# Kernel optimization log

Measured on AMD Instinct MI355X. Metric: run time of the kernel, lower is better.

Reference implementation:

```python
import jax, jax.numpy as jnp
import numpy as np

H = 8
DK = 16  # 128 // 8
DM = 128


def setup_inputs() -> dict:
    key = jax.random.key(0)
    ks = jax.random.split(key, 12)
    B, S = 4, 2048
    inp = {
        "query": jax.random.normal(ks[0], (B, S, DM), dtype=jnp.float32),
        "key": jax.random.normal(ks[1], (B, S, DM), dtype=jnp.float32),
        "value": jax.random.normal(ks[2], (B, S, DM), dtype=jnp.float32),
        "pos_embed": jax.random.normal(ks[3], (B, S, DM), dtype=jnp.float32),
        # three projection linears (shared: L0 for pos_query & query, L1 for pos_key & key, L2 for value)
        "W0": jax.random.normal(ks[4], (DM, DM), dtype=jnp.float32) / np.sqrt(DM),
        "b0": jnp.zeros((DM,), dtype=jnp.float32),
        "W1": jax.random.normal(ks[5], (DM, DM), dtype=jnp.float32) / np.sqrt(DM),
        "b1": jnp.zeros((DM,), dtype=jnp.float32),
        "W2": jax.random.normal(ks[6], (DM, DM), dtype=jnp.float32) / np.sqrt(DM),
        "b2": jnp.zeros((DM,), dtype=jnp.float32),
        "Wo": jax.random.normal(ks[7], (DM, DM), dtype=jnp.float32) / np.sqrt(DM),
        "bo": jnp.zeros((DM,), dtype=jnp.float32),
    }
    return inp


def _proj(x, W, b):
    # Linear then split heads: [B,S,128] -> [B,H,S,DK]
    B = x.shape[0]
    y = x @ W.T + b
    return y.reshape(B, -1, H, DK).transpose(0, 2, 1, 3)


def reference(query, key, value, pos_embed, W0, b0, W1, b1, W2, b2, Wo, bo):
    B = query.shape[0]
    pos1 = pos_embed[..., 0:DM]
    pos_q = _proj(pos1, W0, b0)  # shares L0 with query proj (as in source zip bug)
    pos_k = _proj(pos1, W1, b1)
    pos_attn = jnp.einsum("bhqd,bhkd->bhqk", pos_q, pos_k)  # [B,H,S,S]

    q = _proj(query, W0, b0)
    k = _proj(key, W1, b1)
    v = _proj(value, W2, b2)

    scale = 1.0 / jnp.sqrt(jnp.asarray(DK, dtype=q.dtype))
    scores = jnp.einsum("bhqd,bhkd->bhqk", q, k) * scale + pos_attn
    attn = jax.nn.softmax(scores, axis=-1)  # dropout = identity (eval)
    x = jnp.einsum("bhqk,bhkd->bhqd", attn, v)  # [B,H,S,DK]
    x = x.transpose(0, 2, 1, 3).reshape(B, -1, H * DK)
    return x @ Wo.T + bo
```

## Files before the change

kernel.cpp:

```cpp
#include <hip/hip_runtime.h>
#include <math.h>

#define LOG2E 1.44269504088896340736f

typedef __attribute__((ext_vector_type(8))) short bfrag;
typedef __attribute__((ext_vector_type(4))) float f4;
typedef unsigned __attribute__((ext_vector_type(2))) u2;

__device__ __forceinline__ unsigned pk_trunc(float a, float b) {
    return (__float_as_uint(a) >> 16) | (__float_as_uint(b) & 0xFFFF0000u);
}
__device__ __forceinline__ unsigned pk_rne(float a, float b) {
    unsigned ua = __float_as_uint(a); ua += 0x7FFFu + ((ua >> 16) & 1u);
    unsigned ub = __float_as_uint(b); ub += 0x7FFFu + ((ub >> 16) & 1u);
    return (ua >> 16) | (ub & 0xFFFF0000u);
}
__device__ __forceinline__ float trunchi(float x) {
    return __uint_as_float(__float_as_uint(x) & 0xFFFF0000u);
}
__device__ __forceinline__ float fexp2(float x) {
#if __has_builtin(__builtin_amdgcn_exp2f)
    return __builtin_amdgcn_exp2f(x);
#else
    return exp2f(x);
#endif
}
__device__ __forceinline__ void plswap16(float& a, float& b) {
#if __has_builtin(__builtin_amdgcn_permlane16_swap)
    u2 t = __builtin_amdgcn_permlane16_swap(__float_as_uint(a), __float_as_uint(b),
                                            false, false);
    a = __uint_as_float(t.x); b = __uint_as_float(t.y);
#else
    bool odd = (threadIdx.x >> 4) & 1;
    float bs = __shfl_xor(b, 16, 64);
    float as = __shfl_xor(a, 16, 64);
    float na = odd ? bs : a;
    float nb = odd ? b : as;
    a = na; b = nb;
#endif
}
__device__ __forceinline__ void stage16(void* lds_base, const void* g) {
#if __has_builtin(__builtin_amdgcn_global_load_lds)
    __builtin_amdgcn_global_load_lds(
        (const __attribute__((address_space(1))) unsigned int*)g,
        (__attribute__((address_space(3))) unsigned int*)lds_base, 16, 0, 0);
#else
    int lane = threadIdx.x & 63;
    *(float4*)((char*)lds_base + lane * 16) = *(const float4*)g;
#endif
}
__device__ __forceinline__ f4 mfma_bf16(bfrag a, bfrag b, f4 c) {
    return __builtin_amdgcn_mfma_f32_16x16x32_bf16(a, b, c, 0, 0, 0);
}
__device__ __forceinline__ void conv8(const float* __restrict__ g, bfrag& hi, bfrag& lo) {
    f4 a = *(const f4*)g;
    f4 b = *(const f4*)(g + 4);
    union { unsigned u[4]; bfrag v; } H, L;
    H.u[0] = pk_trunc(a.x, a.y); H.u[1] = pk_trunc(a.z, a.w);
    H.u[2] = pk_trunc(b.x, b.y); H.u[3] = pk_trunc(b.z, b.w);
    L.u[0] = pk_trunc(a.x - trunchi(a.x), a.y - trunchi(a.y));
    L.u[1] = pk_trunc(a.z - trunchi(a.z), a.w - trunchi(a.w));
    L.u[2] = pk_trunc(b.x - trunchi(b.x), b.y - trunchi(b.y));
    L.u[3] = pk_trunc(b.z - trunchi(b.z), b.w - trunchi(b.w));
    hi = H.v; lo = L.v;
}
__device__ __forceinline__ void store_q(f4 ea, f4 eb, char* base, int lodelta, int lane) {
    float eah[4], eal[4], ebh[4], ebl[4];
#pragma unroll
    for (int r = 0; r < 4; ++r) {
        eah[r] = trunchi(ea[r]); eal[r] = ea[r] - eah[r];
        ebh[r] = trunchi(eb[r]); ebl[r] = eb[r] - ebh[r];
    }
#pragma unroll
    for (int r = 0; r < 4; ++r) { plswap16(eah[r], ebh[r]); plswap16(eal[r], ebl[r]); }
    union { unsigned u[4]; bfrag v; } H, L;
    H.u[0] = pk_trunc(eah[0], eah[1]); H.u[1] = pk_trunc(eah[2], eah[3]);
    H.u[2] = pk_trunc(ebh[0], ebh[1]); H.u[3] = pk_trunc(ebh[2], ebh[3]);
    L.u[0] = pk_trunc(eal[0], eal[1]); L.u[1] = pk_trunc(eal[2], eal[3]);
    L.u[2] = pk_trunc(ebl[0], ebl[1]); L.u[3] = pk_trunc(ebl[2], ebl[3]);
    *(bfrag*)(base + lane * 16) = H.v;
    *(bfrag*)(base + lodelta + lane * 16) = L.v;
}
__device__ __forceinline__ void store_rne(f4 ea, f4 eb, char* base, int lane) {
    float a[4], b[4];
#pragma unroll
    for (int r = 0; r < 4; ++r) { a[r] = ea[r]; b[r] = eb[r]; }
#pragma unroll
    for (int r = 0; r < 4; ++r) plswap16(a[r], b[r]);
    union { unsigned u[4]; bfrag v; } P;
    P.u[0] = pk_rne(a[0], a[1]); P.u[1] = pk_rne(a[2], a[3]);
    P.u[2] = pk_rne(b[0], b[1]); P.u[3] = pk_rne(b[2], b[3]);
    *(bfrag*)(base + lane * 16) = P.v;
}

#define WS_QB 0u
#define WS_KV 8388608u
#define WS_X  14680064u
#define WS_WI 18874368u

__global__ __launch_bounds__(256) void w_prep(
    const float* __restrict__ W0, const float* __restrict__ W1,
    const float* __restrict__ W2, const float* __restrict__ Wo,
    char* __restrict__ wimg)
{
    int wid = blockIdx.x * 4 + (threadIdx.x >> 6);
    int lane = threadIdx.x & 63;
    int img = wid >> 5, rem = wid & 31, tile = rem >> 2, kg = rem & 3;
    const float* W = (img <= 1) ? W0 : (img == 2) ? W1 : (img == 3) ? W2 : Wo;
    float s = (img == 0) ? 0.25f * LOG2E : (img == 1) ? LOG2E : 1.0f;
    int n = lane & 15, qd = lane >> 4;
    const float* g = W + (size_t)(tile * 16 + n) * 128 + kg * 32 + qd * 8;
    f4 a = *(const f4*)g, b = *(const f4*)(g + 4);
    a.x *= s; a.y *= s; a.z *= s; a.w *= s;
    b.x *= s; b.y *= s; b.z *= s; b.w *= s;
    union { unsigned u[4]; bfrag v; } H, L;
    H.u[0] = pk_trunc(a.x, a.y); H.u[1] = pk_trunc(a.z, a.w);
    H.u[2] = pk_trunc(b.x, b.y); H.u[3] = pk_trunc(b.z, b.w);
    L.u[0] = pk_trunc(a.x - trunchi(a.x), a.y - trunchi(a.y));
    L.u[1] = pk_trunc(a.z - trunchi(a.z), a.w - trunchi(a.w));
    L.u[2] = pk_trunc(b.x - trunchi(b.x), b.y - trunchi(b.y));
    L.u[3] = pk_trunc(b.z - trunchi(b.z), b.w - trunchi(b.w));
    char* dst = wimg + img * 65536 + tile * 8192 + kg * 2048;
    *(bfrag*)(dst + lane * 16) = H.v;
    *(bfrag*)(dst + 1024 + lane * 16) = L.v;
}

__global__ __launch_bounds__(256) void k_proj(
    const float* __restrict__ query, const float* __restrict__ key,
    const float* __restrict__ value, const float* __restrict__ pos,
    const float* __restrict__ b0, const float* __restrict__ b1,
    const float* __restrict__ b2,
    const char* __restrict__ wimg, char* __restrict__ qb, char* __restrict__ kv)
{
    const int tid = threadIdx.x;
    const int w = tid >> 6, lane = tid & 63;
    const int n = lane & 15, qd = lane >> 4;
    const int bid = blockIdx.x;
    const int bh = bid >> 4, b = bh >> 3, h = bh & 7;
    const int s32 = ((bid & 15) << 2) | w;

    {
        bfrag wqh[4], wql[4], wph[4], wpl[4];
#pragma unroll
        for (int kg = 0; kg < 4; ++kg) {
            const char* wb = wimg + 0 * 65536 + h * 8192 + kg * 2048;
            wqh[kg] = *(const bfrag*)(wb + lane * 16);
            wql[kg] = *(const bfrag*)(wb + 1024 + lane * 16);
            const char* pb = wimg + 1 * 65536 + h * 8192 + kg * 2048;
            wph[kg] = *(const bfrag*)(pb + lane * 16);
            wpl[kg] = *(const bfrag*)(pb + 1024 + lane * 16);
        }
        float bq[4], bp[4];
#pragma unroll
        for (int r = 0; r < 4; ++r) {
            float bv = b0[h * 16 + qd * 4 + r];
            bq[r] = 0.25f * LOG2E * bv; bp[r] = LOG2E * bv;
        }
#pragma unroll
        for (int pp = 0; pp < 2; ++pp) {
            int p = 2 * s32 + pp;
            size_t rowg = (size_t)(b * 2048 + p * 16 + n) * 128 + qd * 8;
            f4 cq = {bq[0], bq[1], bq[2], bq[3]};
            f4 cp = {bp[0], bp[1], bp[2], bp[3]};
#pragma unroll
            for (int kg = 0; kg < 4; ++kg) {
                bfrag xh, xl, ph, pl;
                conv8(query + rowg + kg * 32, xh, xl);
                conv8(pos + rowg + kg * 32, ph, pl);
                cq = mfma_bf16(wqh[kg], xh, cq);
                cq = mfma_bf16(wqh[kg], xl, cq);
                cq = mfma_bf16(wql[kg], xh, cq);
                cp = mfma_bf16(wph[kg], ph, cp);
                cp = mfma_bf16(wph[kg], pl, cp);
                cp = mfma_bf16(wpl[kg], ph, cp);
            }
            store_q(cq, cp, qb + (size_t)bh * 262144 + (size_t)p * 2048, 1024, lane);
        }
    }
    {
        bfrag w1h[4], w1l[4];
#pragma unroll
        for (int kg = 0; kg < 4; ++kg) {
            const char* wb = wimg + 2 * 65536 + h * 8192 + kg * 2048;
            w1h[kg] = *(const bfrag*)(wb + lane * 16);
            w1l[kg] = *(const bfrag*)(wb + 1024 + lane * 16);
        }
        float bk[4];
#pragma unroll
        for (int r = 0; r < 4; ++r) bk[r] = b1[h * 16 + qd * 4 + r];
#pragma unroll
        for (int pp = 0; pp < 2; ++pp) {
            int p = 2 * s32 + pp;
            size_t rowg = (size_t)(b * 2048 + p * 16 + n) * 128 + qd * 8;
            f4 ck = {bk[0], bk[1], bk[2], bk[3]};
            f4 cpk = {bk[0], bk[1], bk[2], bk[3]};
#pragma unroll
            for (int kg = 0; kg < 4; ++kg) {
                bfrag xh, xl, ph, pl;
                conv8(key + rowg + kg * 32, xh, xl);
                conv8(pos + rowg + kg * 32, ph, pl);
                ck = mfma_bf16(w1h[kg], xh, ck);
                ck = mfma_bf16(w1h[kg], xl, ck);
                ck = mfma_bf16(w1l[kg], xh, ck);
                cpk = mfma_bf16(w1h[kg], ph, cpk);
                cpk = mfma_bf16(w1h[kg], pl, cpk);
                cpk = mfma_bf16(w1l[kg], ph, cpk);
            }
            store_rne(ck, cpk,
                      kv + (size_t)bh * 196608 + (size_t)(p >> 3) * 12288 + (p & 7) * 1024,
                      lane);
        }
    }
    {
        bfrag w2h[4], w2l[4];
#pragma unroll
        for (int kg = 0; kg < 4; ++kg) {
            const char* wb = wimg + 3 * 65536 + h * 8192 + kg * 2048;
            w2h[kg] = *(const bfrag*)(wb + lane * 16);
            w2l[kg] = *(const bfrag*)(wb + 1024 + lane * 16);
        }
        float bv = b2[h * 16 + n];
        f4 ca = {bv, bv, bv, bv};
        f4 cb = {bv, bv, bv, bv};
#pragma unroll
        for (int pp = 0; pp < 2; ++pp) {
            size_t rowg = (size_t)(b * 2048 + (2 * s32 + pp) * 16 + n) * 128 + qd * 8;
#pragma unroll
            for (int kg = 0; kg < 4; ++kg) {
                bfrag ah, al;
                conv8(value + rowg + kg * 32, ah, al);
                if (pp == 0) {
                    ca = mfma_bf16(ah, w2h[kg], ca);
                    ca = mfma_bf16(al, w2h[kg], ca);
                    ca = mfma_bf16(ah, w2l[kg], ca);
                } else {
                    cb = mfma_bf16(ah, w2h[kg], cb);
                    cb = mfma_bf16(al, w2h[kg], cb);
                    cb = mfma_bf16(ah, w2l[kg], cb);
                }
            }
        }
        store_rne(ca, cb,
                  kv + (size_t)bh * 196608 + (size_t)(s32 >> 2) * 12288
                  + 8192 + (s32 & 3) * 1024, lane);
    }
}

__global__ __launch_bounds__(256) void k_attn(
    const char* __restrict__ qb, const char* __restrict__ kvg,
    float* __restrict__ xout)
{
    __shared__ __align__(16) char kbuf[2][12288];
    const int tid = threadIdx.x;
    const int w = tid >> 6, lane = tid & 63;
    const int c = lane & 15, qd = lane >> 4;
    const int bh = blockIdx.y;
    const int q0 = blockIdx.x * 128 + w * 32;

    const char* qpb = qb + (size_t)bh * 262144 + (size_t)(q0 >> 4) * 2048;
    bfrag qh0 = *(const bfrag*)(qpb + lane * 16);
    bfrag ql0 = *(const bfrag*)(qpb + 1024 + lane * 16);
    bfrag qh1 = *(const bfrag*)(qpb + 2048 + lane * 16);
    bfrag ql1 = *(const bfrag*)(qpb + 3072 + lane * 16);

    const char* kvb = kvg + (size_t)bh * 196608;

    union { unsigned u[4]; bfrag v; } onesu;
    onesu.u[0] = 0x3F803F80u; onesu.u[1] = 0x3F803F80u;
    onesu.u[2] = 0x3F803F80u; onesu.u[3] = 0x3F803F80u;
    const bfrag ones = onesu.v;

    f4 o0 = {0.f, 0.f, 0.f, 0.f}, o1 = {0.f, 0.f, 0.f, 0.f};
    f4 l0 = {0.f, 0.f, 0.f, 0.f}, l1 = {0.f, 0.f, 0.f, 0.f};

    auto stage = [&](char* db, const char* gsrc) {
        stage16(db + w * 2048, gsrc + w * 2048 + lane * 16);
        stage16(db + w * 2048 + 1024, gsrc + w * 2048 + 1024 + lane * 16);
        stage16(db + 8192 + w * 1024, gsrc + 8192 + w * 1024 + lane * 16);
    };

    stage(kbuf[0], kvb);
    int cur = 0;
    for (int ch = 0; ch < 16; ++ch) {
        asm volatile("s_waitcnt vmcnt(0)" ::: "memory");
        __syncthreads();
        if (ch < 15) stage(kbuf[cur ^ 1], kvb + (size_t)(ch + 1) * 12288);
        const char* kb = kbuf[cur];
#pragma unroll
        for (int sub = 0; sub < 4; ++sub) {
            bfrag ka = *(const bfrag*)(kb + (2 * sub) * 1024 + lane * 16);
            bfrag kc2 = *(const bfrag*)(kb + (2 * sub + 1) * 1024 + lane * 16);
            bfrag vf = *(const bfrag*)(kb + 8192 + sub * 1024 + lane * 16);
            {
                f4 sa = {0.f, 0.f, 0.f, 0.f}, sb = {0.f, 0.f, 0.f, 0.f};
                sa = mfma_bf16(ka, qh0, sa);  sa = mfma_bf16(ka, ql0, sa);
                sb = mfma_bf16(kc2, qh0, sb); sb = mfma_bf16(kc2, ql0, sb);
                float ea[4], eb[4];
#pragma unroll
                for (int r = 0; r < 4; ++r) { ea[r] = fexp2(sa[r]); eb[r] = fexp2(sb[r]); }
#pragma unroll
                for (int r = 0; r < 4; ++r) plswap16(ea[r], eb[r]);
                union { unsigned u[4]; bfrag v; } pf;
                pf.u[0] = pk_trunc(ea[0], ea[1]); pf.u[1] = pk_trunc(ea[2], ea[3]);
                pf.u[2] = pk_trunc(eb[0], eb[1]); pf.u[3] = pk_trunc(eb[2], eb[3]);
                o0 = mfma_bf16(pf.v, vf, o0);
                l0 = mfma_bf16(pf.v, ones, l0);
            }
            {
                f4 sa = {0.f, 0.f, 0.f, 0.f}, sb = {0.f, 0.f, 0.f, 0.f};
                sa = mfma_bf16(ka, qh1, sa);  sa = mfma_bf16(ka, ql1, sa);
                sb = mfma_bf16(kc2, qh1, sb); sb = mfma_bf16(kc2, ql1, sb);
                float ea[4], eb[4];
#pragma unroll
                for (int r = 0; r < 4; ++r) { ea[r] = fexp2(sa[r]); eb[r] = fexp2(sb[r]); }
#pragma unroll
                for (int r = 0; r < 4; ++r) plswap16(ea[r], eb[r]);
                union { unsigned u[4]; bfrag v; } pf;
                pf.u[0] = pk_trunc(ea[0], ea[1]); pf.u[1] = pk_trunc(ea[2], ea[3]);
                pf.u[2] = pk_trunc(eb[0], eb[1]); pf.u[3] = pk_trunc(eb[2], eb[3]);
                o1 = mfma_bf16(pf.v, vf, o1);
                l1 = mfma_bf16(pf.v, ones, l1);
            }
        }
        cur ^= 1;
    }

    const int bbk = bh >> 3, h = bh & 7;
#pragma unroll
    for (int r = 0; r < 4; ++r) {
        int row = qd * 4 + r;
        xout[((size_t)(bbk * 2048 + q0 + row)) * 128 + h * 16 + c] = o0[r] / l0[r];
        xout[((size_t)(bbk * 2048 + q0 + 16 + row)) * 128 + h * 16 + c] = o1[r] / l1[r];
    }
}

__global__ __launch_bounds__(128) void k_out(
    const float* __restrict__ x, const char* __restrict__ wimg,
    const float* __restrict__ bo, float* __restrict__ out)
{
    const int tid = threadIdx.x;
    const int w = tid >> 6, lane = tid & 63;
    const int n = lane & 15, qd = lane >> 4;
    const int row0 = (blockIdx.x * 2 + w) * 16;

    bfrag xh[4], xl[4];
#pragma unroll
    for (int kg = 0; kg < 4; ++kg)
        conv8(x + (size_t)(row0 + n) * 128 + kg * 32 + qd * 8, xh[kg], xl[kg]);

#pragma unroll
    for (int t = 0; t < 8; ++t) {
        float bv = bo[t * 16 + n];
        f4 cacc = {bv, bv, bv, bv};
#pragma unroll
        for (int kg = 0; kg < 4; ++kg) {
            const char* wb = wimg + 4 * 65536 + t * 8192 + kg * 2048;
            bfrag wh = *(const bfrag*)(wb + lane * 16);
            bfrag wl = *(const bfrag*)(wb + 1024 + lane * 16);
            cacc = mfma_bf16(xh[kg], wh, cacc);
            cacc = mfma_bf16(xl[kg], wh, cacc);
            cacc = mfma_bf16(xh[kg], wl, cacc);
        }
#pragma unroll
        for (int r = 0; r < 4; ++r)
            out[(size_t)(row0 + qd * 4 + r) * 128 + t * 16 + n] = cacc[r];
    }
}

extern "C" void kernel_launch(void* const* d_in, const int* in_sizes, int n_in,
                              void* d_out, int out_size, void* d_ws, size_t ws_size,
                              hipStream_t stream)
{
    const float* query = (const float*)d_in[0];
    const float* key   = (const float*)d_in[1];
    const float* value = (const float*)d_in[2];
    const float* pos   = (const float*)d_in[3];
    const float* W0 = (const float*)d_in[4];
    const float* b0 = (const float*)d_in[5];
    const float* W1 = (const float*)d_in[6];
    const float* b1 = (const float*)d_in[7];
    const float* W2 = (const float*)d_in[8];
    const float* b2 = (const float*)d_in[9];
    const float* Wo = (const float*)d_in[10];
    const float* bo = (const float*)d_in[11];

    char* ws = (char*)d_ws;
    char* qbuf = ws + WS_QB;
    char* kv   = ws + WS_KV;
    float* x   = (float*)(ws + WS_X);
    char* wimg = ws + WS_WI;
    float* out = (float*)d_out;

    w_prep<<<dim3(40), 256, 0, stream>>>(W0, W1, W2, Wo, wimg);
    k_proj<<<dim3(512), 256, 0, stream>>>(query, key, value, pos, b0, b1, b2,
                                          wimg, qbuf, kv);
    k_attn<<<dim3(16, 32), 256, 0, stream>>>(qbuf, kv, x);
    k_out<<<dim3(256), 128, 0, stream>>>(x, wimg, bo, out);
}
```

Before: 144.6 us.

## Stage projection inputs in LDS once per row tile and share across heads

The projection kernel now has each block load and convert a 32-row tile of query/key/value/pos into bf16 hi/lo fragments in 64KB of shared memory once. Its four waves each then handle two heads, where previously every head re-read and re-converted the same rows from global memory. The output kernel splits its column tiles across the two waves so it launches twice as many blocks, pk_trunc uses a byte-permute builtin, and the attention loop advances its prefetch pointer incrementally. The large LDS allocation limits occupancy, and the grid for the projection kernel is halved.

```diff
diff --git a/kernel.cpp b/kernel.cpp
--- a/kernel.cpp
+++ b/kernel.cpp
@@ -8,7 +8,11 @@
 typedef unsigned __attribute__((ext_vector_type(2))) u2;
 
 __device__ __forceinline__ unsigned pk_trunc(float a, float b) {
+#if __has_builtin(__builtin_amdgcn_perm)
+    return __builtin_amdgcn_perm(__float_as_uint(b), __float_as_uint(a), 0x07060302u);
+#else
     return (__float_as_uint(a) >> 16) | (__float_as_uint(b) & 0xFFFF0000u);
+#endif
 }
 __device__ __forceinline__ unsigned pk_rne(float a, float b) {
     unsigned ua = __float_as_uint(a); ua += 0x7FFFu + ((ua >> 16) & 1u);
@@ -132,117 +136,138 @@
     const float* __restrict__ b2,
     const char* __restrict__ wimg, char* __restrict__ qb, char* __restrict__ kv)
 {
+    __shared__ __align__(16) char xlds[65536];
     const int tid = threadIdx.x;
+    const int bid = blockIdx.x;
+    const int b = bid >> 6, s32 = bid & 63;
+    const size_t rowbase = (size_t)(b * 2048 + s32 * 32);
+
+#pragma unroll
+    for (int i = 0; i < 8; ++i) {
+        int cid = tid + i * 256;
+        int arr = cid >> 9, rem = cid & 511;
+        int c32 = rem >> 4, u = rem & 15;
+        const float* sp = (arr == 0) ? query : (arr == 1) ? key
+                        : (arr == 2) ? value : pos;
+        bfrag hi, lo;
+        conv8(sp + (rowbase + c32) * 128 + u * 8, hi, lo);
+        int base = arr * 16384 + (c32 >> 4) * 8192 + (u >> 2) * 2048
+                 + ((u & 3) * 16 + (c32 & 15)) * 16;
+        *(bfrag*)(xlds + base) = hi;
+        *(bfrag*)(xlds + base + 1024) = lo;
+    }
+    __syncthreads();
+
     const int w = tid >> 6, lane = tid & 63;
     const int n = lane & 15, qd = lane >> 4;
-    const int bid = blockIdx.x;
-    const int bh = bid >> 4, b = bh >> 3, h = bh & 7;
-    const int s32 = ((bid & 15) << 2) | w;
-
-    {
-        bfrag wqh[4], wql[4], wph[4], wpl[4];
-#pragma unroll
-        for (int kg = 0; kg < 4; ++kg) {
-            const char* wb = wimg + 0 * 65536 + h * 8192 + kg * 2048;
-            wqh[kg] = *(const bfrag*)(wb + lane * 16);
-            wql[kg] = *(const bfrag*)(wb + 1024 + lane * 16);
-            const char* pb = wimg + 1 * 65536 + h * 8192 + kg * 2048;
-            wph[kg] = *(const bfrag*)(pb + lane * 16);
-            wpl[kg] = *(const bfrag*)(pb + 1024 + lane * 16);
+#pragma unroll
+    for (int hh = 0; hh < 2; ++hh) {
+        const int h = w * 2 + hh;
+        const int bh = b * 8 + h;
+        {
+            bfrag wqh[4], wql[4], wph[4], wpl[4];
+#pragma unroll
+            for (int kg = 0; kg < 4; ++kg) {
+                const char* wb = wimg + 0 * 65536 + h * 8192 + kg * 2048;
+                wqh[kg] = *(const bfrag*)(wb + lane * 16);
+                wql[kg] = *(const bfrag*)(wb + 1024 + lane * 16);
+                const char* pb = wimg + 1 * 65536 + h * 8192 + kg * 2048;
+                wph[kg] = *(const bfrag*)(pb + lane * 16);
+                wpl[kg] = *(const bfrag*)(pb + 1024 + lane * 16);
+            }
+            float bq[4], bp[4];
+#pragma unroll
+            for (int r = 0; r < 4; ++r) {
+                float bv = b0[h * 16 + qd * 4 + r];
+                bq[r] = 0.25f * LOG2E * bv; bp[r] = LOG2E * bv;
+            }
+#pragma unroll
+            for (int pp = 0; pp < 2; ++pp) {
+                f4 cq = {bq[0], bq[1], bq[2], bq[3]};
+                f4 cp = {bp[0], bp[1], bp[2], bp[3]};
+#pragma unroll
+                for (int kg = 0; kg < 4; ++kg) {
+                    const char* xq = xlds + 0 * 16384 + pp * 8192 + kg * 2048 + lane * 16;
+                    const char* xp = xlds + 3 * 16384 + pp * 8192 + kg * 2048 + lane * 16;
+                    bfrag xh = *(const bfrag*)xq, xl = *(const bfrag*)(xq + 1024);
+                    bfrag ph = *(const bfrag*)xp, pl = *(const bfrag*)(xp + 1024);
+                    cq = mfma_bf16(wqh[kg], xh, cq);
+                    cq = mfma_bf16(wqh[kg], xl, cq);
+                    cq = mfma_bf16(wql[kg], xh, cq);
+                    cp = mfma_bf16(wph[kg], ph, cp);
+                    cp = mfma_bf16(wph[kg], pl, cp);
+                    cp = mfma_bf16(wpl[kg], ph, cp);
+                }
+                int pg = s32 * 2 + pp;
+                store_q(cq, cp, qb + (size_t)bh * 262144 + (size_t)pg * 2048, 1024, lane);
+            }
         }
-        float bq[4], bp[4];
-#pragma unroll
-        for (int r = 0; r < 4; ++r) {
-            float bv = b0[h * 16 + qd * 4 + r];
-            bq[r] = 0.25f * LOG2E * bv; bp[r] = LOG2E * bv;
+        {
+            bfrag w1h[4], w1l[4];
+#pragma unroll
+            for (int kg = 0; kg < 4; ++kg) {
+                const char* wb = wimg + 2 * 65536 + h * 8192 + kg * 2048;
+                w1h[kg] = *(const bfrag*)(wb + lane * 16);
+                w1l[kg] = *(const bfrag*)(wb + 1024 + lane * 16);
+            }
+            float bk[4];
+#pragma unroll
+            for (int r = 0; r < 4; ++r) bk[r] = b1[h * 16 + qd * 4 + r];
+#pragma unroll
+            for (int pp = 0; pp < 2; ++pp) {
+                f4 ck = {bk[0], bk[1], bk[2], bk[3]};
+                f4 cpk = {bk[0], bk[1], bk[2], bk[3]};
+#pragma unroll
+                for (int kg = 0; kg < 4; ++kg) {
+                    const char* xk = xlds + 1 * 16384 + pp * 8192 + kg * 2048 + lane * 16;
+                    const char* xp = xlds + 3 * 16384 + pp * 8192 + kg * 2048 + lane * 16;
+                    bfrag xh = *(const bfrag*)xk, xl = *(const bfrag*)(xk + 1024);
+                    bfrag ph = *(const bfrag*)xp, pl = *(const bfrag*)(xp + 1024);
+                    ck = mfma_bf16(w1h[kg], xh, ck);
+                    ck = mfma_bf16(w1h[kg], xl, ck);
+                    ck = mfma_bf16(w1l[kg], xh, ck);
+                    cpk = mfma_bf16(w1h[kg], ph, cpk);
+                    cpk = mfma_bf16(w1h[kg], pl, cpk);
+                    cpk = mfma_bf16(w1l[kg], ph, cpk);
+                }
+                int pg = s32 * 2 + pp;
+                store_rne(ck, cpk,
+                          kv + (size_t)bh * 196608 + (size_t)(pg >> 3) * 12288
+                          + (pg & 7) * 1024, lane);
+            }
         }
-#pragma unroll
-        for (int pp = 0; pp < 2; ++pp) {
-            int p = 2 * s32 + pp;
-            size_t rowg = (size_t)(b * 2048 + p * 16 + n) * 128 + qd * 8;
-            f4 cq = {bq[0], bq[1], bq[2], bq[3]};
-            f4 cp = {bp[0], bp[1], bp[2], bp[3]};
+        {
+            bfrag w2h[4], w2l[4];
 #pragma unroll
             for (int kg = 0; kg < 4; ++kg) {
-                bfrag xh, xl, ph, pl;
-                conv8(query + rowg + kg * 32, xh, xl);
-                conv8(pos + rowg + kg * 32, ph, pl);
-                cq = mfma_bf16(wqh[kg], xh, cq);
-                cq = mfma_bf16(wqh[kg], xl, cq);
-                cq = mfma_bf16(wql[kg], xh, cq);
-                cp = mfma_bf16(wph[kg], ph, cp);
-                cp = mfma_bf16(wph[kg], pl, cp);
-                cp = mfma_bf16(wpl[kg], ph, cp);
-            }
-            store_q(cq, cp, qb + (size_t)bh * 262144 + (size_t)p * 2048, 1024, lane);
+                const char* wb = wimg + 3 * 65536 + h * 8192 + kg * 2048;
+                w2h[kg] = *(const bfrag*)(wb + lane * 16);
+                w2l[kg] = *(const bfrag*)(wb + 1024 + lane * 16);
+            }
+            float bv = b2[h * 16 + n];
+            f4 ca = {bv, bv, bv, bv};
+            f4 cb = {bv, bv, bv, bv};
+#pragma unroll
+            for (int pp = 0; pp < 2; ++pp) {
+#pragma unroll
+                for (int kg = 0; kg < 4; ++kg) {
+                    const char* xv = xlds + 2 * 16384 + pp * 8192 + kg * 2048 + lane * 16;
+                    bfrag ah = *(const bfrag*)xv, al = *(const bfrag*)(xv + 1024);
+                    if (pp == 0) {
+                        ca = mfma_bf16(ah, w2h[kg], ca);
+                        ca = mfma_bf16(al, w2h[kg], ca);
+                        ca = mfma_bf16(ah, w2l[kg], ca);
+                    } else {
+                        cb = mfma_bf16(ah, w2h[kg], cb);
+                        cb = mfma_bf16(al, w2h[kg], cb);
+                        cb = mfma_bf16(ah, w2l[kg], cb);
+                    }
+                }
+            }
+            store_rne(ca, cb,
+                      kv + (size_t)bh * 196608 + (size_t)(s32 >> 2) * 12288
+                      + 8192 + (s32 & 3) * 1024, lane);
         }
-    }
-    {
-        bfrag w1h[4], w1l[4];
-#pragma unroll
-        for (int kg = 0; kg < 4; ++kg) {
-            const char* wb = wimg + 2 * 65536 + h * 8192 + kg * 2048;
-            w1h[kg] = *(const bfrag*)(wb + lane * 16);
-            w1l[kg] = *(const bfrag*)(wb + 1024 + lane * 16);
-        }
-        float bk[4];
-#pragma unroll
-        for (int r = 0; r < 4; ++r) bk[r] = b1[h * 16 + qd * 4 + r];
-#pragma unroll
-        for (int pp = 0; pp < 2; ++pp) {
-            int p = 2 * s32 + pp;
-            size_t rowg = (size_t)(b * 2048 + p * 16 + n) * 128 + qd * 8;
-            f4 ck = {bk[0], bk[1], bk[2], bk[3]};
-            f4 cpk = {bk[0], bk[1], bk[2], bk[3]};
-#pragma unroll
-            for (int kg = 0; kg < 4; ++kg) {
-                bfrag xh, xl, ph, pl;
-                conv8(key + rowg + kg * 32, xh, xl);
-                conv8(pos + rowg + kg * 32, ph, pl);
-                ck = mfma_bf16(w1h[kg], xh, ck);
-                ck = mfma_bf16(w1h[kg], xl, ck);
-                ck = mfma_bf16(w1l[kg], xh, ck);
-                cpk = mfma_bf16(w1h[kg], ph, cpk);
-                cpk = mfma_bf16(w1h[kg], pl, cpk);
-                cpk = mfma_bf16(w1l[kg], ph, cpk);
-            }
-            store_rne(ck, cpk,
-                      kv + (size_t)bh * 196608 + (size_t)(p >> 3) * 12288 + (p & 7) * 1024,
-                      lane);
-        }
-    }
-    {
-        bfrag w2h[4], w2l[4];
-#pragma unroll
-        for (int kg = 0; kg < 4; ++kg) {
-            const char* wb = wimg + 3 * 65536 + h * 8192 + kg * 2048;
-            w2h[kg] = *(const bfrag*)(wb + lane * 16);
-            w2l[kg] = *(const bfrag*)(wb + 1024 + lane * 16);
-        }
-        float bv = b2[h * 16 + n];
-        f4 ca = {bv, bv, bv, bv};
-        f4 cb = {bv, bv, bv, bv};
-#pragma unroll
-        for (int pp = 0; pp < 2; ++pp) {
-            size_t rowg = (size_t)(b * 2048 + (2 * s32 + pp) * 16 + n) * 128 + qd * 8;
-#pragma unroll
-            for (int kg = 0; kg < 4; ++kg) {
-                bfrag ah, al;
-                conv8(value + rowg + kg * 32, ah, al);
-                if (pp == 0) {
-                    ca = mfma_bf16(ah, w2h[kg], ca);
-                    ca = mfma_bf16(al, w2h[kg], ca);
-                    ca = mfma_bf16(ah, w2l[kg], ca);
-                } else {
-                    cb = mfma_bf16(ah, w2h[kg], cb);
-                    cb = mfma_bf16(al, w2h[kg], cb);
-                    cb = mfma_bf16(ah, w2l[kg], cb);
-                }
-            }
-        }
-        store_rne(ca, cb,
-                  kv + (size_t)bh * 196608 + (size_t)(s32 >> 2) * 12288
-                  + 8192 + (s32 & 3) * 1024, lane);
     }
 }
 
@@ -280,11 +305,12 @@
     };
 
     stage(kbuf[0], kvb);
+    const char* gnext = kvb + 12288;
     int cur = 0;
     for (int ch = 0; ch < 16; ++ch) {
         asm volatile("s_waitcnt vmcnt(0)" ::: "memory");
         __syncthreads();
-        if (ch < 15) stage(kbuf[cur ^ 1], kvb + (size_t)(ch + 1) * 12288);
+        if (ch < 15) { stage(kbuf[cur ^ 1], gnext); gnext += 12288; }
         const char* kb = kbuf[cur];
 #pragma unroll
         for (int sub = 0; sub < 4; ++sub) {
@@ -341,7 +367,7 @@
     const int tid = threadIdx.x;
     const int w = tid >> 6, lane = tid & 63;
     const int n = lane & 15, qd = lane >> 4;
-    const int row0 = (blockIdx.x * 2 + w) * 16;
+    const int row0 = blockIdx.x * 16;
 
     bfrag xh[4], xl[4];
 #pragma unroll
@@ -349,7 +375,8 @@
         conv8(x + (size_t)(row0 + n) * 128 + kg * 32 + qd * 8, xh[kg], xl[kg]);
 
 #pragma unroll
-    for (int t = 0; t < 8; ++t) {
+    for (int tt = 0; tt < 4; ++tt) {
+        int t = w * 4 + tt;
         float bv = bo[t * 16 + n];
         f4 cacc = {bv, bv, bv, bv};
 #pragma unroll
@@ -392,8 +419,8 @@
     float* out = (float*)d_out;
 
     w_prep<<<dim3(40), 256, 0, stream>>>(W0, W1, W2, Wo, wimg);
-    k_proj<<<dim3(512), 256, 0, stream>>>(query, key, value, pos, b0, b1, b2,
+    k_proj<<<dim3(256), 256, 0, stream>>>(query, key, value, pos, b0, b1, b2,
                                           wimg, qbuf, kv);
     k_attn<<<dim3(16, 32), 256, 0, stream>>>(qbuf, kv, x);
-    k_out<<<dim3(256), 128, 0, stream>>>(x, wimg, bo, out);
-}
+    k_out<<<dim3(512), 128, 0, stream>>>(x, wimg, bo, out);
+}
```

Result: faster. 132.2 us (-8.6%).
